# Optimization experiments

Measured on AMD Instinct MI355X. Metric: run time of the kernel, lower is better.

## Reference

```python
import jax, jax.numpy as jnp
import numpy as np

N_HEADS = 16
HEAD_SZ = 64

def setup_inputs() -> dict:
    key = jax.random.key(0)
    ks = jax.random.split(key, 6)
    E = 1024
    s = 1.0 / np.sqrt(E)
    return {
        "x": jax.random.normal(ks[0], (2, 2048, E), dtype=jnp.float32),
        "Wq": jax.random.normal(ks[1], (E, N_HEADS * HEAD_SZ), dtype=jnp.float32) * s,
        "Wk": jax.random.normal(ks[2], (E, N_HEADS * HEAD_SZ), dtype=jnp.float32) * s,
        "Wv": jax.random.normal(ks[3], (E, N_HEADS * HEAD_SZ), dtype=jnp.float32) * s,
        "Wp": jax.random.normal(ks[4], (N_HEADS * HEAD_SZ, E), dtype=jnp.float32) * s,
        "bp": jnp.zeros((E,), dtype=jnp.float32),
    }

def reference(x, Wq, Wk, Wv, Wp, bp):
    # flavor="masked": causal self-attention, pdrop=0 -> dropout is identity
    B, S, E = x.shape
    H, D = N_HEADS, HEAD_SZ
    q = (x @ Wq).reshape(B, S, H, D).transpose(0, 2, 1, 3)  # [B,H,S,D]
    k = (x @ Wk).reshape(B, S, H, D).transpose(0, 2, 1, 3)
    v = (x @ Wv).reshape(B, S, H, D).transpose(0, 2, 1, 3)
    scores = jnp.einsum("bhqd,bhkd->bhqk", q, k) / jnp.sqrt(jnp.float32(D))
    causal = jnp.tril(jnp.ones((S, S), dtype=bool))  # [S,S]
    scores = jnp.where(causal, scores, -jnp.inf)
    attn = jax.nn.softmax(scores, axis=-1)
    out = jnp.einsum("bhqk,bhkd->bhqd", attn, v)  # [B,H,S,D]
    out = out.transpose(0, 2, 1, 3).reshape(B, S, H * D)
    return out @ Wp + bp
```

## Files before the change

### kernel.cpp

```cpp
#include <hip/hip_runtime.h>
#include <hip/hip_bf16.h>
#include <math.h>

using bf16 = __hip_bfloat16;
typedef __attribute__((ext_vector_type(8))) short short8;
typedef __attribute__((ext_vector_type(4))) float floatx4;

#define MFMA16(a, b, c) __builtin_amdgcn_mfma_f32_16x16x32_bf16((a), (b), (c), 0, 0, 0)

__device__ __forceinline__ void gll16(const void* g, void* l) {
  __builtin_amdgcn_global_load_lds((__attribute__((address_space(1))) void*)(uintptr_t)g,
                                   (__attribute__((address_space(3))) void*)l, 16, 0, 0);
}

__global__ void detect_bias_k(const unsigned short* __restrict__ x,
                              const void* __restrict__ bsrc,
                              bf16* __restrict__ bdst, int* __restrict__ flag) {
  __shared__ int cnt;
  if (threadIdx.x == 0) cnt = 0;
  __syncthreads();
  int local = 0;
  for (int i = threadIdx.x; i < 8192; i += 256) {
    unsigned short v = x[2 * i];
    if (((v >> 7) & 0xFF) == 0xFF) local++;
  }
  if (local) atomicAdd(&cnt, local);
  __syncthreads();
  int f = (cnt > 0) ? 1 : 0;
  if (threadIdx.x == 0) *flag = f;
  for (int i = threadIdx.x; i < 1024; i += 256)
    bdst[i] = f ? __float2bfloat16(((const float*)bsrc)[i]) : ((const bf16*)bsrc)[i];
}

__global__ __launch_bounds__(256) void prep_k(const void* __restrict__ xin,
                                              bf16* __restrict__ xb,
                                              const void* __restrict__ W0,
                                              const void* __restrict__ W1,
                                              const void* __restrict__ W2,
                                              const void* __restrict__ W3,
                                              bf16* __restrict__ Wt,
                                              bf16* __restrict__ Wpt,
                                              const int* __restrict__ flag) {
  bool f32 = (*flag != 0);
  int z = blockIdx.z;
  if (z < 2) {
    int tid = threadIdx.y * 32 + threadIdx.x;
    int blockLin = z * 1024 + blockIdx.y * 32 + blockIdx.x;
    int idx = blockLin * 2048 + tid * 8;
    if (f32) {
      const float4* p = reinterpret_cast<const float4*>((const float*)xin + idx);
      float4 a = p[0], b = p[1];
      union { bf16 h[8]; uint4 u; } U;
      U.h[0] = __float2bfloat16(a.x); U.h[1] = __float2bfloat16(a.y);
      U.h[2] = __float2bfloat16(a.z); U.h[3] = __float2bfloat16(a.w);
      U.h[4] = __float2bfloat16(b.x); U.h[5] = __float2bfloat16(b.y);
      U.h[6] = __float2bfloat16(b.z); U.h[7] = __float2bfloat16(b.w);
      *reinterpret_cast<uint4*>(xb + idx) = U.u;
    } else {
      *reinterpret_cast<uint4*>(xb + idx) =
          *reinterpret_cast<const uint4*>((const bf16*)xin + idx);
    }
    return;
  }
  const void* src = (z == 2) ? W0 : (z == 3) ? W1 : (z == 4) ? W2 : W3;
  bf16* dst = (z == 5) ? Wpt : (Wt + (size_t)(z - 2) * 1024 * 1024);
  __shared__ float tsh[32][33];
  int tx = threadIdx.x, ty = threadIdx.y;
  int k0 = blockIdx.y * 32, n0 = blockIdx.x * 32;
  for (int i = 0; i < 4; i++) {
    size_t off = (size_t)(k0 + ty + i * 8) * 1024 + n0 + tx;
    tsh[ty + i * 8][tx] = f32 ? ((const float*)src)[off]
                              : __bfloat162float(((const bf16*)src)[off]);
  }
  __syncthreads();
  for (int i = 0; i < 4; i++)
    dst[(size_t)(n0 + ty + i * 8) * 1024 + k0 + tx] = __float2bfloat16(tsh[tx][ty + i * 8]);
}

__global__ __launch_bounds__(512) void vtrans_k(const bf16* __restrict__ QKV,
                                                bf16* __restrict__ VT) {
  __shared__ bf16 t[64][66];
  int tx = threadIdx.x, ty = threadIdx.y;
  int s0 = blockIdx.x * 64, bh = blockIdx.y;
  int b = bh >> 4, h = bh & 15;
  size_t rowb = (size_t)b * 2048;
  int hv = 2048 + h * 64;
#pragma unroll
  for (int i = 0; i < 8; i++)
    t[i * 8 + ty][tx] = QKV[(rowb + s0 + i * 8 + ty) * 3072 + hv + tx];
  __syncthreads();
#pragma unroll
  for (int i = 0; i < 8; i++)
    VT[((size_t)bh * 64 + i * 8 + ty) * 2048 + s0 + tx] = t[tx][i * 8 + ty];
}

__global__ __launch_bounds__(256) void gemm_bt128(const bf16* __restrict__ A, int lda,
                                                  const bf16* __restrict__ Bt, int ldb,
                                                  void* __restrict__ C, int ldc,
                                                  const bf16* __restrict__ bias, int K,
                                                  const int* __restrict__ outflag) {
  __shared__ bf16 As[2][128 * 32];
  __shared__ bf16 Bs[2][128 * 32];
  int t = threadIdx.x;
  int w = t >> 6, lane = t & 63;
  int g = lane >> 4, c = lane & 15;
  int wm = (w >> 1) * 64, wn = (w & 1) * 64;
  int m0 = blockIdx.y * 128, n0 = blockIdx.x * 128;

  int sr = w * 32 + (lane >> 2);
  int sc = (lane & 3) * 8;
  const bf16* Ab = A + (size_t)(m0 + sr) * lda + sc;
  const bf16* Bb = Bt + (size_t)(n0 + sr) * ldb + sc;
  int lofs = (w * 32) * 32;

  floatx4 acc[4][4] = {};

  for (int k0 = 0; k0 < K; k0 += 64) {
    __syncthreads();
#pragma unroll
    for (int h = 0; h < 2; h++) {
      gll16(Ab + k0 + h * 32, &As[h][lofs]);
      gll16(Ab + k0 + h * 32 + (size_t)16 * lda, &As[h][lofs + 16 * 32]);
      gll16(Bb + k0 + h * 32, &Bs[h][lofs]);
      gll16(Bb + k0 + h * 32 + (size_t)16 * ldb, &Bs[h][lofs + 16 * 32]);
    }
    __syncthreads();
#pragma unroll
    for (int h = 0; h < 2; h++) {
      short8 af[4], bf[4];
#pragma unroll
      for (int i = 0; i < 4; i++) {
        af[i] = *reinterpret_cast<const short8*>(&As[h][(wm + i * 16 + c) * 32 + g * 8]);
        bf[i] = *reinterpret_cast<const short8*>(&Bs[h][(wn + i * 16 + c) * 32 + g * 8]);
      }
#pragma unroll
      for (int i = 0; i < 4; i++)
#pragma unroll
        for (int j = 0; j < 4; j++) acc[i][j] = MFMA16(af[i], bf[j], acc[i][j]);
    }
  }

  bool f32out = (outflag != nullptr) && (*outflag != 0);
#pragma unroll
  for (int i = 0; i < 4; i++) {
    int rbase = m0 + wm + i * 16 + g * 4;
#pragma unroll
    for (int j = 0; j < 4; j++) {
      int col = n0 + wn + j * 16 + c;
      float bv = bias ? __bfloat162float(bias[col]) : 0.f;
#pragma unroll
      for (int r = 0; r < 4; r++) {
        size_t off = (size_t)(rbase + r) * ldc + col;
        float v = acc[i][j][r] + bv;
        if (f32out) ((float*)C)[off] = v;
        else ((bf16*)C)[off] = __float2bfloat16(v);
      }
    }
  }
}

__global__ __launch_bounds__(256) void gemm_bt64(const bf16* __restrict__ A, int lda,
                                                 const bf16* __restrict__ Bt, int ldb,
                                                 void* __restrict__ C, int ldc,
                                                 const bf16* __restrict__ bias, int K,
                                                 const int* __restrict__ outflag) {
  __shared__ bf16 As[2][128 * 32];
  __shared__ bf16 Bs[2][64 * 32];
  int t = threadIdx.x;
  int w = t >> 6, lane = t & 63;
  int g = lane >> 4, c = lane & 15;
  int wm = (w >> 1) * 64, wn = (w & 1) * 32;
  int m0 = blockIdx.y * 128, n0 = blockIdx.x * 64;

  int sr = (lane >> 2);
  int sc = (lane & 3) * 8;
  const bf16* Ab = A + (size_t)(m0 + w * 32 + sr) * lda + sc;
  const bf16* Bb = Bt + (size_t)(n0 + w * 16 + sr) * ldb + sc;
  int laofs = (w * 32) * 32;
  int lbofs = (w * 16) * 32;

  floatx4 acc[4][2] = {};

  for (int k0 = 0; k0 < K; k0 += 64) {
    __syncthreads();
#pragma unroll
    for (int h = 0; h < 2; h++) {
      gll16(Ab + k0 + h * 32, &As[h][laofs]);
      gll16(Ab + k0 + h * 32 + (size_t)16 * lda, &As[h][laofs + 16 * 32]);
      gll16(Bb + k0 + h * 32, &Bs[h][lbofs]);
    }
    __syncthreads();
#pragma unroll
    for (int h = 0; h < 2; h++) {
      short8 af[4], bf[2];
#pragma unroll
      for (int i = 0; i < 4; i++)
        af[i] = *reinterpret_cast<const short8*>(&As[h][(wm + i * 16 + c) * 32 + g * 8]);
#pragma unroll
      for (int j = 0; j < 2; j++)
        bf[j] = *reinterpret_cast<const short8*>(&Bs[h][(wn + j * 16 + c) * 32 + g * 8]);
#pragma unroll
      for (int i = 0; i < 4; i++)
#pragma unroll
        for (int j = 0; j < 2; j++) acc[i][j] = MFMA16(af[i], bf[j], acc[i][j]);
    }
  }

  bool f32out = (outflag != nullptr) && (*outflag != 0);
#pragma unroll
  for (int i = 0; i < 4; i++) {
    int rbase = m0 + wm + i * 16 + g * 4;
#pragma unroll
    for (int j = 0; j < 2; j++) {
      int col = n0 + wn + j * 16 + c;
      float bv = bias ? __bfloat162float(bias[col]) : 0.f;
#pragma unroll
      for (int r = 0; r < 4; r++) {
        size_t off = (size_t)(rbase + r) * ldc + col;
        float v = acc[i][j][r] + bv;
        if (f32out) ((float*)C)[off] = v;
        else ((bf16*)C)[off] = __float2bfloat16(v);
      }
    }
  }
}

__global__ __launch_bounds__(512, 4) void attn_lds2(bf16* __restrict__ QKV,
                                                    const bf16* __restrict__ VT) {
  const int S = 2048, LD = 3072;
  __shared__ bf16 Ks[2][2][64 * 32];
  __shared__ bf16 Vs[2][2][64 * 32];
  __shared__ bf16 Pb[8][16 * 72];

  int t = threadIdx.x, w = t >> 6, lane = t & 63, g = lane >> 4, c = lane & 15;

  int r = blockIdx.x + 16 * blockIdx.y;
  int xcd = r & 7;
  int s = r >> 3;
  int bh = xcd + 8 * (s >> 4);
  int u = s & 15;
  int qt = (u & 1) ? (15 - (u >> 1)) : (u >> 1);

  int b = bh >> 4, h = bh & 15;
  int qbase = qt * 128;
  size_t rowb = (size_t)b * S;
  int hq = h * 64, hk = 1024 + h * 64;
  const bf16* Vt = VT + (size_t)bh * 64 * 2048;
  bf16* pb = Pb[w];

  int su = (w & 3) * 16 + (lane >> 2);
  int sc = (lane & 3) * 8;
  const bf16* Kg = &QKV[(rowb + su) * LD + hk + sc];
  const bf16* Vg = &Vt[(size_t)su * 2048 + sc];
  int sofs = ((w & 3) * 16) * 32;

  short8 qf[2];
#pragma unroll
  for (int hf = 0; hf < 2; hf++)
    qf[hf] = *reinterpret_cast<const short8*>(
        &QKV[(rowb + qbase + w * 16 + c) * LD + hq + hf * 32 + g * 8]);

  floatx4 o[4] = {};
  float lsum = 0.f;
  int qrow = qbase + w * 16 + c;

  int nkt = 2 * qt + 2;
  if (w < 4) {
    gll16(Kg, &Ks[0][0][sofs]);
    gll16(Kg + 32, &Ks[0][1][sofs]);
  } else {
    gll16(Vg, &Vs[0][0][sofs]);
    gll16(Vg + 32, &Vs[0][1][sofs]);
  }

  for (int kt = 0; kt < nkt; kt++) {
    int kbase = kt * 64;
    int cur = kt & 1;
    __syncthreads();
    if (kt + 1 < nkt) {
      int nb = cur ^ 1;
      size_t kofs = (size_t)(kbase + 64);
      if (w < 4) {
        gll16(Kg + kofs * LD, &Ks[nb][0][sofs]);
        gll16(Kg + kofs * LD + 32, &Ks[nb][1][sofs]);
      } else {
        gll16(Vg + kofs, &Vs[nb][0][sofs]);
        gll16(Vg + kofs + 32, &Vs[nb][1][sofs]);
      }
    }

    short8 kf[4][2];
#pragma unroll
    for (int nt = 0; nt < 4; nt++)
#pragma unroll
      for (int hf = 0; hf < 2; hf++)
        kf[nt][hf] =
            *reinterpret_cast<const short8*>(&Ks[cur][hf][(nt * 16 + c) * 32 + g * 8]);

    floatx4 sv[4];
    __builtin_amdgcn_s_setprio(1);
#pragma unroll
    for (int nt = 0; nt < 4; nt++) {
      floatx4 z = {};
      z = MFMA16(kf[nt][0], qf[0], z);
      z = MFMA16(kf[nt][1], qf[1], z);
      sv[nt] = z;
    }
    __builtin_amdgcn_s_setprio(0);

    bool diag = (kbase + 63 > qbase + w * 16);
#pragma unroll
    for (int nt = 0; nt < 4; nt++) {
      int kcol0 = kbase + nt * 16 + g * 4;
#pragma unroll
      for (int rr = 0; rr < 4; rr++) {
        float arg = fmaf(sv[nt][rr], 0.18033688f, -23.083120f);
        if (diag && (kcol0 + rr > qrow)) arg = -1e30f;
        float p = exp2f(arg);
        lsum += p;
        sv[nt][rr] = p;
      }
    }

#pragma unroll
    for (int nt = 0; nt < 4; nt++) {
      union { bf16 h4[4]; uint2 u2; } U;
      U.h4[0] = __float2bfloat16(sv[nt][0]);
      U.h4[1] = __float2bfloat16(sv[nt][1]);
      U.h4[2] = __float2bfloat16(sv[nt][2]);
      U.h4[3] = __float2bfloat16(sv[nt][3]);
      *reinterpret_cast<uint2*>(&pb[c * 72 + nt * 16 + g * 4]) = U.u2;
    }
    asm volatile("s_waitcnt lgkmcnt(0)" ::: "memory");
    short8 pf0 = *reinterpret_cast<const short8*>(&pb[c * 72 + g * 8]);
    short8 pf1 = *reinterpret_cast<const short8*>(&pb[c * 72 + 32 + g * 8]);

    __builtin_amdgcn_s_setprio(1);
#pragma unroll
    for (int dt = 0; dt < 4; dt++) {
      short8 vf0 = *reinterpret_cast<const short8*>(&Vs[cur][0][(dt * 16 + c) * 32 + g * 8]);
      short8 vf1 = *reinterpret_cast<const short8*>(&Vs[cur][1][(dt * 16 + c) * 32 + g * 8]);
      o[dt] = MFMA16(pf0, vf0, o[dt]);
      o[dt] = MFMA16(pf1, vf1, o[dt]);
    }
    __builtin_amdgcn_s_setprio(0);
  }

  lsum += __shfl_xor(lsum, 16);
  lsum += __shfl_xor(lsum, 32);
  float lrec = 1.0f / lsum;
  float l_r[4];
#pragma unroll
  for (int rr = 0; rr < 4; rr++) l_r[rr] = __shfl(lrec, g * 4 + rr);

#pragma unroll
  for (int dt = 0; dt < 4; dt++)
#pragma unroll
    for (int rr = 0; rr < 4; rr++) {
      float v = o[dt][rr] * l_r[rr];
      QKV[(rowb + qbase + w * 16 + g * 4 + rr) * LD + hq + dt * 16 + c] =
          __float2bfloat16(v);
    }
}

extern "C" void kernel_launch(void* const* d_in, const int* in_sizes, int n_in,
                              void* d_out, int out_size, void* d_ws, size_t ws_size,
                              hipStream_t stream) {
  char* ws = (char*)d_ws;
  const size_t MB = 1024 * 1024;
  int* flag = (int*)ws;
  bf16* bias = (bf16*)(ws + 4096);
  bf16* xb = (bf16*)(ws + 1 * MB);
  bf16* Wt = (bf16*)(ws + 9 * MB);
  bf16* Wpt = (bf16*)(ws + 15 * MB);
  bf16* QKV = (bf16*)(ws + 17 * MB);
  bf16* VT = xb;

  detect_bias_k<<<1, 256, 0, stream>>>((const unsigned short*)d_in[0], d_in[5], bias, flag);
  prep_k<<<dim3(32, 32, 6), dim3(32, 8), 0, stream>>>(d_in[0], xb, d_in[1], d_in[2],
                                                      d_in[3], d_in[4], Wt, Wpt, flag);

  gemm_bt128<<<dim3(24, 32), 256, 0, stream>>>(xb, 1024, Wt, 1024, QKV, 3072, nullptr,
                                               1024, nullptr);
  vtrans_k<<<dim3(32, 32), dim3(64, 8), 0, stream>>>(QKV, VT);
  attn_lds2<<<dim3(16, 32), 512, 0, stream>>>(QKV, VT);
  gemm_bt64<<<dim3(16, 32), 256, 0, stream>>>(QKV, 3072, Wpt, 1024, d_out, 1024, bias,
                                              1024, flag);
}
```

Before: 221.6 us.

## Split long causal attention tiles across two blocks and combine partials

Query tiles 8-15, which have the most key blocks, are split in half along the key dimension. The two halves run as separate blocks that write unnormalized fp32 partial outputs and row sums. A new combine kernel adds the halves and normalizes them. Lookup tables assign the 768 blocks so that each group of three carries roughly equal causal work. This is meant to even out load across CUs and shorten the tail, at the cost of an extra launch, extra fp32 traffic, and borrowing d_out as scratch space.

```diff
diff --git a/kernel.cpp b/kernel.cpp
--- a/kernel.cpp
+++ b/kernel.cpp
@@ -225,8 +225,15 @@
   }
 }
 
+__device__ const int QT_TAB[8][3] = {{15, 15, 0}, {7, 13, 1},  {14, 12, 2}, {14, 10, 3},
+                                     {13, 4, 9},  {6, 10, 8},  {12, 11, 8}, {5, 11, 9}};
+__device__ const int HF_TAB[8][3] = {{0, 1, 2}, {2, 0, 2}, {0, 0, 2}, {1, 0, 2},
+                                     {1, 2, 0}, {2, 1, 0}, {1, 0, 1}, {2, 1, 1}};
+
 __global__ __launch_bounds__(512, 4) void attn_lds2(bf16* __restrict__ QKV,
-                                                    const bf16* __restrict__ VT) {
+                                                    const bf16* __restrict__ VT,
+                                                    float* __restrict__ Po,
+                                                    float* __restrict__ Pl) {
   const int S = 2048, LD = 3072;
   __shared__ bf16 Ks[2][2][64 * 32];
   __shared__ bf16 Vs[2][2][64 * 32];
@@ -234,12 +241,16 @@
 
   int t = threadIdx.x, w = t >> 6, lane = t & 63, g = lane >> 4, c = lane & 15;
 
-  int r = blockIdx.x + 16 * blockIdx.y;
+  int r = blockIdx.x + 24 * blockIdx.y;
   int xcd = r & 7;
   int s = r >> 3;
-  int bh = xcd + 8 * (s >> 4);
-  int u = s & 15;
-  int qt = (u & 1) ? (15 - (u >> 1)) : (u >> 1);
+  int r3 = s >> 5;
+  int u = s & 31;
+  int hg = u >> 3;
+  int tri = u & 7;
+  int bh = xcd + 8 * hg;
+  int qt = QT_TAB[tri][r3];
+  int hf = HF_TAB[tri][r3];
 
   int b = bh >> 4, h = bh & 15;
   int qbase = qt * 128;
@@ -248,6 +259,10 @@
   const bf16* Vt = VT + (size_t)bh * 64 * 2048;
   bf16* pb = Pb[w];
 
+  int nkt = 2 * qt + 2;
+  int kb0 = (hf == 1) ? (qt + 1) : 0;
+  int kb1 = (hf == 0) ? (qt + 1) : nkt;
+
   int su = (w & 3) * 16 + (lane >> 2);
   int sc = (lane & 3) * 8;
   const bf16* Kg = &QKV[(rowb + su) * LD + hk + sc];
@@ -256,28 +271,30 @@
 
   short8 qf[2];
 #pragma unroll
-  for (int hf = 0; hf < 2; hf++)
-    qf[hf] = *reinterpret_cast<const short8*>(
-        &QKV[(rowb + qbase + w * 16 + c) * LD + hq + hf * 32 + g * 8]);
+  for (int hfr = 0; hfr < 2; hfr++)
+    qf[hfr] = *reinterpret_cast<const short8*>(
+        &QKV[(rowb + qbase + w * 16 + c) * LD + hq + hfr * 32 + g * 8]);
 
   floatx4 o[4] = {};
   float lsum = 0.f;
   int qrow = qbase + w * 16 + c;
 
-  int nkt = 2 * qt + 2;
-  if (w < 4) {
-    gll16(Kg, &Ks[0][0][sofs]);
-    gll16(Kg + 32, &Ks[0][1][sofs]);
-  } else {
-    gll16(Vg, &Vs[0][0][sofs]);
-    gll16(Vg + 32, &Vs[0][1][sofs]);
-  }
-
-  for (int kt = 0; kt < nkt; kt++) {
+  {
+    size_t k0off = (size_t)kb0 * 64;
+    if (w < 4) {
+      gll16(Kg + k0off * LD, &Ks[0][0][sofs]);
+      gll16(Kg + k0off * LD + 32, &Ks[0][1][sofs]);
+    } else {
+      gll16(Vg + k0off, &Vs[0][0][sofs]);
+      gll16(Vg + k0off + 32, &Vs[0][1][sofs]);
+    }
+  }
+
+  for (int kt = kb0; kt < kb1; kt++) {
     int kbase = kt * 64;
-    int cur = kt & 1;
+    int cur = (kt - kb0) & 1;
     __syncthreads();
-    if (kt + 1 < nkt) {
+    if (kt + 1 < kb1) {
       int nb = cur ^ 1;
       size_t kofs = (size_t)(kbase + 64);
       if (w < 4) {
@@ -293,9 +310,9 @@
 #pragma unroll
     for (int nt = 0; nt < 4; nt++)
 #pragma unroll
-      for (int hf = 0; hf < 2; hf++)
-        kf[nt][hf] =
-            *reinterpret_cast<const short8*>(&Ks[cur][hf][(nt * 16 + c) * 32 + g * 8]);
+      for (int hfr = 0; hfr < 2; hfr++)
+        kf[nt][hfr] =
+            *reinterpret_cast<const short8*>(&Ks[cur][hfr][(nt * 16 + c) * 32 + g * 8]);
 
     floatx4 sv[4];
     __builtin_amdgcn_s_setprio(1);
@@ -348,19 +365,54 @@
 
   lsum += __shfl_xor(lsum, 16);
   lsum += __shfl_xor(lsum, 32);
-  float lrec = 1.0f / lsum;
-  float l_r[4];
-#pragma unroll
-  for (int rr = 0; rr < 4; rr++) l_r[rr] = __shfl(lrec, g * 4 + rr);
-
-#pragma unroll
-  for (int dt = 0; dt < 4; dt++)
-#pragma unroll
-    for (int rr = 0; rr < 4; rr++) {
-      float v = o[dt][rr] * l_r[rr];
-      QKV[(rowb + qbase + w * 16 + g * 4 + rr) * LD + hq + dt * 16 + c] =
-          __float2bfloat16(v);
-    }
+
+  if (hf == 2) {
+    float lrec = 1.0f / lsum;
+    float l_r[4];
+#pragma unroll
+    for (int rr = 0; rr < 4; rr++) l_r[rr] = __shfl(lrec, g * 4 + rr);
+#pragma unroll
+    for (int dt = 0; dt < 4; dt++)
+#pragma unroll
+      for (int rr = 0; rr < 4; rr++) {
+        float v = o[dt][rr] * l_r[rr];
+        QKV[(rowb + qbase + w * 16 + g * 4 + rr) * LD + hq + dt * 16 + c] =
+            __float2bfloat16(v);
+      }
+  } else {
+    int slot = (bh * 8 + (qt - 8)) * 2 + hf;
+    float* po = Po + (size_t)slot * (128 * 64);
+    float* pl = Pl + slot * 128;
+    if (g == 0) pl[w * 16 + c] = lsum;
+#pragma unroll
+    for (int dt = 0; dt < 4; dt++)
+#pragma unroll
+      for (int rr = 0; rr < 4; rr++)
+        po[(w * 16 + g * 4 + rr) * 64 + dt * 16 + c] = o[dt][rr];
+  }
+}
+
+__global__ __launch_bounds__(256) void combine_k(const float* __restrict__ Po,
+                                                 const float* __restrict__ Pl,
+                                                 bf16* __restrict__ QKV) {
+  int qi = blockIdx.x;
+  int bh = blockIdx.y;
+  int b = bh >> 4, h = bh & 15;
+  int qt = 8 + qi;
+  int slot = (bh * 8 + qi) * 2;
+  const float* oA = Po + (size_t)slot * (128 * 64);
+  const float* oB = oA + 128 * 64;
+  const float* lA = Pl + slot * 128;
+  const float* lB = lA + 128;
+  int t = threadIdx.x;
+#pragma unroll
+  for (int i = 0; i < 32; i++) {
+    int idx = t + i * 256;
+    int row = idx >> 6, d = idx & 63;
+    float l = lA[row] + lB[row];
+    float v = (oA[idx] + oB[idx]) / l;
+    QKV[((size_t)b * 2048 + qt * 128 + row) * 3072 + h * 64 + d] = __float2bfloat16(v);
+  }
 }
 
 extern "C" void kernel_launch(void* const* d_in, const int* in_sizes, int n_in,
@@ -375,6 +427,9 @@
   bf16* Wpt = (bf16*)(ws + 15 * MB);
   bf16* QKV = (bf16*)(ws + 17 * MB);
   bf16* VT = xb;
+  float* Pl = (float*)(ws + 41 * MB);
+  float* Po = (out_size >= (int)(16 * MB)) ? (float*)d_out
+                                           : (float*)(ws + 42 * MB);
 
   detect_bias_k<<<1, 256, 0, stream>>>((const unsigned short*)d_in[0], d_in[5], bias, flag);
   prep_k<<<dim3(32, 32, 6), dim3(32, 8), 0, stream>>>(d_in[0], xb, d_in[1], d_in[2],
@@ -383,7 +438,8 @@
   gemm_bt128<<<dim3(24, 32), 256, 0, stream>>>(xb, 1024, Wt, 1024, QKV, 3072, nullptr,
                                                1024, nullptr);
   vtrans_k<<<dim3(32, 32), dim3(64, 8), 0, stream>>>(QKV, VT);
-  attn_lds2<<<dim3(16, 32), 512, 0, stream>>>(QKV, VT);
+  attn_lds2<<<dim3(24, 32), 512, 0, stream>>>(QKV, VT, Po, Pl);
+  combine_k<<<dim3(8, 32), 256, 0, stream>>>(Po, Pl, QKV);
   gemm_bt64<<<dim3(16, 32), 256, 0, stream>>>(QKV, 3072, Wpt, 1024, d_out, 1024, bias,
                                               1024, flag);
 }
```

After: 197.6 us (median of 2 runs). 1.12x faster.
